# Kernel optimization log

Hardware: AMD Instinct MI355X
Metric: run time of the kernel (lower is better)

The kernel has to match this reference:

```python
import jax, jax.numpy as jnp
import numpy as np
from itertools import permutations

NODE, BATCH, DIM, STEP = 32, 64, 32, 8
E = NODE * (NODE - 1)          # 992 directed edges (all ordered pairs)
K = 3                          # edge types
MSG_HID = 64; MSG_OUT = 64; N_HID = 64; PRED_LEN = 8


def setup_inputs() -> dict:
    key = jax.random.key(0)
    ks = jax.random.split(key, 12)
    es = jnp.asarray(np.array(list(permutations(range(NODE), 2))).T, dtype=jnp.int32)  # [2, E]
    x = jax.random.normal(ks[0], (BATCH, NODE, DIM, STEP), jnp.float32)
    z = jax.nn.softmax(jax.random.normal(ks[1], (BATCH, E, K), jnp.float32), axis=-1)
    p = lambda k, shape: jax.random.normal(k, shape, jnp.float32) * 0.1
    return dict(
        x=x, z=z, es=es,
        nodes_mask=jnp.zeros((NODE,), jnp.float32),
        edges_mask=jnp.zeros((E,), jnp.float32),
        mask=jnp.zeros((1,), jnp.float32),
        msg_W1=p(ks[2], (K, 2 * DIM, MSG_HID)), msg_b1=jnp.zeros((K, MSG_HID), jnp.float32),
        msg_W2=p(ks[3], (K, MSG_HID, MSG_OUT)), msg_b2=jnp.zeros((K, MSG_OUT), jnp.float32),
        out_W1=p(ks[4], (DIM + MSG_OUT, N_HID)), out_b1=jnp.zeros((N_HID,), jnp.float32),
        out_W2=p(ks[5], (N_HID, N_HID)), out_b2=jnp.zeros((N_HID,), jnp.float32),
        out_W3=p(ks[6], (N_HID, DIM)), out_b3=jnp.zeros((DIM,), jnp.float32),
        ge_Wi=p(ks[7], (3, N_HID, N_HID)), ge_bi=jnp.zeros((3, N_HID), jnp.float32),
        ge_Wh=p(ks[8], (3, N_HID, N_HID)), ge_bh=jnp.zeros((3, N_HID), jnp.float32),
        gn_Wi=p(ks[9], (3, N_HID + DIM, N_HID + DIM)), gn_bi=jnp.zeros((3, N_HID + DIM), jnp.float32),
        gn_Wh=p(ks[10], (3, N_HID + DIM, N_HID + DIM)), gn_bh=jnp.zeros((3, N_HID + DIM), jnp.float32),
    )


def _gru(inp, hid, Wi, bi, Wh, bh):
    # GRUX: state defaults to hidden
    r = jax.nn.sigmoid(inp @ Wi[0] + bi[0] + hid @ Wh[0] + bh[0])
    i = jax.nn.sigmoid(inp @ Wi[1] + bi[1] + hid @ Wh[1] + bh[1])
    n = jnp.tanh(inp @ Wi[2] + bi[2] + r * (hid @ Wh[2] + bh[2]))
    return (1.0 - i) * n + i * hid


def _run(x, z, es, msg_W1, msg_b1, msg_W2, msg_b2,
         out_W1, out_b1, out_W2, out_b2, out_W3, out_b3,
         ge_Wi, ge_bi, ge_Wh, ge_bh, gn_Wi, gn_bi, gn_Wh, gn_bh):
    xp = jnp.transpose(x, (1, 0, 3, 2))   # [node, batch, step, dim]
    zp = jnp.transpose(z, (1, 0, 2))      # [E, batch, K]
    col, row = es[0], es[1]               # 'o2i': col,row = es; aggregate at col
    counts = jnp.clip(jax.ops.segment_sum(jnp.ones((E,), x.dtype), col, num_segments=NODE), 1.0)
    h_node = h_edge = None
    x_m = None
    xs = []
    for t in range(STEP + PRED_LEN):
        x_in = xp[:, :, t, :] if t < STEP else x_m   # [node, batch, dim]
        # edge gather: msg = cat([x[row], x[col]])
        msg = jnp.concatenate([x_in[row], x_in[col]], axis=-1)  # [E, b, 2*dim]
        # per-edge-type 2-layer MLP mixture, weighted by z, normalized by K
        h1 = jax.nn.relu(jnp.einsum('ebi,kih->kebh', msg, msg_W1) + msg_b1[:, None, None, :])
        h2 = jax.nn.relu(jnp.einsum('kebh,kho->kebo', h1, msg_W2) + msg_b2[:, None, None, :])
        msgs = jnp.einsum('kebo,ebk->ebo', h2, zp) / K          # [E, b, msg_out]
        if h_edge is not None:
            msgs = _gru(msgs, h_edge, ge_Wi, ge_bi, ge_Wh, ge_bh)
        # scatter-mean to nodes
        agg = jax.ops.segment_sum(msgs, col, num_segments=NODE) / counts[:, None, None]
        cat = jnp.concatenate([x_in, agg], axis=-1)             # [node, b, dim+msg_out]
        if h_node is not None:
            cat = _gru(cat, h_node, gn_Wi, gn_bi, gn_Wh, gn_bh)
        h = jax.nn.relu(cat @ out_W1 + out_b1)
        h = jax.nn.relu(h @ out_W2 + out_b2)
        delta = h @ out_W3 + out_b3
        x_m = x_in + delta
        h_node, h_edge = cat, msgs
        xs.append(x_m)
    x_hat = jnp.transpose(jnp.stack(xs, axis=2), (1, 0, 3, 2))  # [batch, node, dim, T]
    return x_hat


def reference(x, z, es, nodes_mask, edges_mask, mask,
              msg_W1, msg_b1, msg_W2, msg_b2,
              out_W1, out_b1, out_W2, out_b2, out_W3, out_b3,
              ge_Wi, ge_bi, ge_Wh, ge_bh, gn_Wi, gn_bi, gn_Wh, gn_bh):
    x_hat = _run(x, z, es, msg_W1, msg_b1, msg_W2, msg_b2,
                 out_W1, out_b1, out_W2, out_b2, out_W3, out_b3,
                 ge_Wi, ge_bi, ge_Wh, ge_bh, gn_Wi, gn_bi, gn_Wh, gn_bh)
    return (x_hat[:, :, :, -PRED_LEN:], x_hat, x_hat)
```

## Files before the change

kernel.cpp:

```cpp
#include <hip/hip_runtime.h>
#include <hip/hip_bf16.h>

#define NNODE 32
#define NB    64
#define NDIM  32
#define NSTEP 8
#define NE    992
#define NTT   16

typedef __bf16 bf16;
typedef __attribute__((ext_vector_type(8))) __bf16 bf16x8;
typedef __attribute__((ext_vector_type(4))) __bf16 bf16x4;
typedef __attribute__((ext_vector_type(4))) float  f32x4;

__device__ __forceinline__ f32x4 mfma_bf16(bf16x8 a, bf16x8 b, f32x4 c) {
  return __builtin_amdgcn_mfma_f32_16x16x32_bf16(a, b, c, 0, 0, 0);
}
__device__ __forceinline__ float sigm(float x) { return 1.0f / (1.0f + __expf(-x)); }
__device__ __forceinline__ float tanh_f(float x) {
  x = fminf(fmaxf(x, -15.0f), 15.0f);
  float e = __expf(2.0f * x);
  return (e - 1.0f) / (e + 1.0f);
}

__global__ void prep_weights(
    const float* __restrict__ msgW1, const float* __restrict__ msgW2,
    const float* __restrict__ geWi,  const float* __restrict__ geWh,
    const float* __restrict__ gnWi,  const float* __restrict__ gnWh,
    const float* __restrict__ oW1,   const float* __restrict__ oW2,
    const float* __restrict__ oW3,
    bf16* __restrict__ B1, bf16* __restrict__ B2,
    bf16* __restrict__ GI, bf16* __restrict__ GH,
    bf16* __restrict__ GN,
    bf16* __restrict__ OW1s, bf16* __restrict__ OW2s, bf16* __restrict__ OW3s) {
  int u = blockIdx.x * 256 + threadIdx.x;
  if (u < 12288) {
    int k = u >> 12, i = (u >> 6) & 63, h = u & 63;
    int kf = i >> 5, quad = (i >> 3) & 3, j = i & 7;
    int nn = k * 64 + h, nt = nn >> 4, lane = quad * 16 + (nn & 15);
    int slot = ((nt * 2 + kf) * 64 + lane) * 8 + j;
    B1[slot] = (bf16)msgW1[u];
    GI[slot] = (bf16)geWi[u];
    GH[slot] = (bf16)geWh[u];
    int ntl = h >> 4, lane2 = quad * 16 + (h & 15);
    int slot2 = k * 4096 + ((ntl * 2 + kf) * 64 + lane2) * 8 + j;
    B2[slot2] = (bf16)msgW2[u];
  } else if (u < 39936) {
    int v = u - 12288;
    int kk = v / 9216, rem = v % 9216, i = rem / 96, h = rem % 96;
    int kf = i >> 5, loc = i & 31, quad = loc >> 3, j = loc & 7;
    int nn = kk * 96 + h, nt = nn >> 4, lane = quad * 16 + (nn & 15);
    int slot = ((nt * 3 + kf) * 64 + lane) * 8 + j;
    GN[slot]         = (bf16)gnWi[v];
    GN[27648 + slot] = (bf16)gnWh[v];
  } else if (u < 46080) {
    int v = u - 39936; int i = v >> 6, h = v & 63;
    int kf = i >> 5, loc = i & 31, quad = loc >> 3, j = loc & 7;
    int nt = h >> 4, lane = quad * 16 + (h & 15);
    OW1s[((nt * 3 + kf) * 64 + lane) * 8 + j] = (bf16)oW1[v];
  } else if (u < 50176) {
    int v = u - 46080; int i = v >> 6, h = v & 63;
    int kf = i >> 5, quad = (i >> 3) & 3, j = i & 7;
    int nt = h >> 4, lane = quad * 16 + (h & 15);
    OW2s[((nt * 2 + kf) * 64 + lane) * 8 + j] = (bf16)oW2[v];
  } else if (u < 52224) {
    int v = u - 50176; int i = v >> 5, h = v & 31;
    int kf = i >> 5, quad = (i >> 3) & 3, j = i & 7;
    int nt = h >> 4, lane = quad * 16 + (h & 15);
    OW3s[((nt * 2 + kf) * 64 + lane) * 8 + j] = (bf16)oW3[v];
  }
}

__global__ void copy_x(const float* __restrict__ x, float* __restrict__ xf,
                       bf16* __restrict__ xb) {
  int u = blockIdx.x * 256 + threadIdx.x;
  int n = u >> 11, b = (u >> 5) & 63, d = u & 31;
  float v = x[((b * 32 + n) * 32 + d) * 8 + 0];
  xf[u] = v;
  xb[u] = (bf16)v;
}

__global__ __launch_bounds__(256, 2) void edge_step(
    const bf16* __restrict__ xb, const int* __restrict__ es,
    const float* __restrict__ z,
    const bf16* __restrict__ B1, const bf16* __restrict__ B2,
    const float* __restrict__ mb1, const float* __restrict__ mb2,
    const bf16* __restrict__ GI, const bf16* __restrict__ GH,
    const float* __restrict__ gbi, const float* __restrict__ gbh,
    bf16* __restrict__ hed, int t) {
  __shared__ __align__(16) char scrbuf[51200];
  __shared__ float zL[2][64][3];
  __shared__ float biasL[768];
  bf16 (*A)[64][72]   = (bf16(*)[64][72])scrbuf;
  bf16 (*A2)[64][200] = (bf16(*)[64][200])scrbuf;

  int e0 = blockIdx.x * 2, tid = threadIdx.x;
  int c0_ = es[e0],     r0 = es[NE + e0];
  int c1_ = es[e0 + 1], r1 = es[NE + e0 + 1];
  for (int u = tid; u < 768; u += 256)
    biasL[u] = (u < 192) ? mb1[u] : (u < 384) ? mb2[u - 192]
             : (u < 576) ? gbi[u - 384] : gbh[u - 576];
  for (int u = tid; u < 384; u += 256) {
    int pe = u / 192, rem = u % 192, b = rem / 3, k = rem % 3;
    zL[pe][b][k] = z[(b * NE + e0 + pe) * 3 + k];
  }
  for (int u = tid; u < 1024; u += 256) {
    int pe = u >> 9, c = u & 511;
    int b = c >> 3, i8 = c & 7;
    int nrow = pe ? r1 : r0, ncol = pe ? c1_ : c0_;
    const bf16* src = (i8 < 4) ? (xb + nrow * 2048 + b * 32 + i8 * 8)
                               : (xb + ncol * 2048 + b * 32 + (i8 - 4) * 8);
    *(bf16x8*)&A[pe][b][i8 * 8] = *(const bf16x8*)src;
  }
  __syncthreads();
  int wv = tid >> 6, ln = tid & 63, quad = ln >> 4, l16 = ln & 15;
  int m = wv * 16 + l16;
  bf16x8 af[2][2];
#pragma unroll
  for (int pe = 0; pe < 2; pe++)
#pragma unroll
    for (int kf = 0; kf < 2; kf++)
      af[pe][kf] = *(const bf16x8*)&A[pe][m][kf * 32 + quad * 8];
  __syncthreads();
  f32x4 acc[2][12];
#pragma unroll
  for (int pe = 0; pe < 2; pe++)
#pragma unroll
    for (int q = 0; q < 12; q++) { f32x4 zz = {0.f,0.f,0.f,0.f}; acc[pe][q] = zz; }
#pragma unroll
  for (int nt = 0; nt < 12; nt++) {
    bf16x8 w0 = *(const bf16x8*)&B1[(nt * 2 + 0) * 512 + ln * 8];
    bf16x8 w1 = *(const bf16x8*)&B1[(nt * 2 + 1) * 512 + ln * 8];
#pragma unroll
    for (int pe = 0; pe < 2; pe++) {
      acc[pe][nt] = mfma_bf16(af[pe][0], w0, acc[pe][nt]);
      acc[pe][nt] = mfma_bf16(af[pe][1], w1, acc[pe][nt]);
    }
  }
#pragma unroll
  for (int nt = 0; nt < 12; nt++) {
    int n = nt * 16 + l16;
    float bias = biasL[n];
#pragma unroll
    for (int pe = 0; pe < 2; pe++)
#pragma unroll
      for (int r = 0; r < 4; r++) {
        float v = acc[pe][nt][r] + bias;
        A2[pe][wv * 16 + quad * 4 + r][n] = (bf16)(v > 0.f ? v : 0.f);
      }
  }
  __syncthreads();
  bf16x8 a2[2][3][2];
#pragma unroll
  for (int pe = 0; pe < 2; pe++)
#pragma unroll
    for (int kt = 0; kt < 3; kt++)
#pragma unroll
      for (int kf = 0; kf < 2; kf++)
        a2[pe][kt][kf] = *(const bf16x8*)&A2[pe][m][kt * 64 + kf * 32 + quad * 8];
  __syncthreads();
  f32x4 acc2[2][12];
#pragma unroll
  for (int pe = 0; pe < 2; pe++)
#pragma unroll
    for (int q = 0; q < 12; q++) { f32x4 zz = {0.f,0.f,0.f,0.f}; acc2[pe][q] = zz; }
#pragma unroll
  for (int kt = 0; kt < 3; kt++)
#pragma unroll
    for (int nt = 0; nt < 4; nt++) {
      bf16x8 w0 = *(const bf16x8*)&B2[kt * 4096 + (nt * 2 + 0) * 512 + ln * 8];
      bf16x8 w1 = *(const bf16x8*)&B2[kt * 4096 + (nt * 2 + 1) * 512 + ln * 8];
#pragma unroll
      for (int pe = 0; pe < 2; pe++) {
        acc2[pe][kt * 4 + nt] = mfma_bf16(a2[pe][kt][0], w0, acc2[pe][kt * 4 + nt]);
        acc2[pe][kt * 4 + nt] = mfma_bf16(a2[pe][kt][1], w1, acc2[pe][kt * 4 + nt]);
      }
    }
#pragma unroll
  for (int pe = 0; pe < 2; pe++)
#pragma unroll
    for (int r = 0; r < 4; r++) {
      int b = wv * 16 + quad * 4 + r;
      float z0 = zL[pe][b][0], z1 = zL[pe][b][1], z2 = zL[pe][b][2];
#pragma unroll
      for (int nt = 0; nt < 4; nt++) {
        int o = nt * 16 + l16;
        float h0 = acc2[pe][nt][r]     + biasL[192 + o];       h0 = h0 > 0.f ? h0 : 0.f;
        float h1 = acc2[pe][4 + nt][r] + biasL[192 + 64 + o];  h1 = h1 > 0.f ? h1 : 0.f;
        float h2 = acc2[pe][8 + nt][r] + biasL[192 + 128 + o]; h2 = h2 > 0.f ? h2 : 0.f;
        A[pe][b][o] = (bf16)((h0 * z0 + h1 * z1 + h2 * z2) * (1.0f / 3.0f));
      }
    }
  if (t > 0) {
    __syncthreads();
    bf16x8 ai[2][2], ah[2][2];
#pragma unroll
    for (int pe = 0; pe < 2; pe++) {
      const bf16* hrow = hed + (e0 + pe) * 4096 + m * 64;
#pragma unroll
      for (int kf = 0; kf < 2; kf++) {
        ai[pe][kf] = *(const bf16x8*)&A[pe][m][kf * 32 + quad * 8];
        ah[pe][kf] = *(const bf16x8*)(hrow + kf * 32 + quad * 8);
      }
    }
    f32x4 gri[2][8], gni[2][4], gnh[2][4];
#pragma unroll
    for (int pe = 0; pe < 2; pe++) {
#pragma unroll
      for (int q = 0; q < 8; q++) { f32x4 zz = {0.f,0.f,0.f,0.f}; gri[pe][q] = zz; }
#pragma unroll
      for (int q = 0; q < 4; q++) { f32x4 zz = {0.f,0.f,0.f,0.f}; gni[pe][q] = zz; gnh[pe][q] = zz; }
    }
#pragma unroll
    for (int nt = 0; nt < 8; nt++) {
      bf16x8 wi0 = *(const bf16x8*)&GI[(nt * 2 + 0) * 512 + ln * 8];
      bf16x8 wi1 = *(const bf16x8*)&GI[(nt * 2 + 1) * 512 + ln * 8];
      bf16x8 wh0 = *(const bf16x8*)&GH[(nt * 2 + 0) * 512 + ln * 8];
      bf16x8 wh1 = *(const bf16x8*)&GH[(nt * 2 + 1) * 512 + ln * 8];
#pragma unroll
      for (int pe = 0; pe < 2; pe++) {
        gri[pe][nt] = mfma_bf16(ai[pe][0], wi0, gri[pe][nt]);
        gri[pe][nt] = mfma_bf16(ai[pe][1], wi1, gri[pe][nt]);
        gri[pe][nt] = mfma_bf16(ah[pe][0], wh0, gri[pe][nt]);
        gri[pe][nt] = mfma_bf16(ah[pe][1], wh1, gri[pe][nt]);
      }
    }
#pragma unroll
    for (int nt = 8; nt < 12; nt++) {
      bf16x8 wi0 = *(const bf16x8*)&GI[(nt * 2 + 0) * 512 + ln * 8];
      bf16x8 wi1 = *(const bf16x8*)&GI[(nt * 2 + 1) * 512 + ln * 8];
      bf16x8 wh0 = *(const bf16x8*)&GH[(nt * 2 + 0) * 512 + ln * 8];
      bf16x8 wh1 = *(const bf16x8*)&GH[(nt * 2 + 1) * 512 + ln * 8];
#pragma unroll
      for (int pe = 0; pe < 2; pe++) {
        gni[pe][nt - 8] = mfma_bf16(ai[pe][0], wi0, gni[pe][nt - 8]);
        gni[pe][nt - 8] = mfma_bf16(ai[pe][1], wi1, gni[pe][nt - 8]);
        gnh[pe][nt - 8] = mfma_bf16(ah[pe][0], wh0, gnh[pe][nt - 8]);
        gnh[pe][nt - 8] = mfma_bf16(ah[pe][1], wh1, gnh[pe][nt - 8]);
      }
    }
#pragma unroll
    for (int pe = 0; pe < 2; pe++)
#pragma unroll
      for (int r = 0; r < 4; r++) {
        int b = wv * 16 + quad * 4 + r;
#pragma unroll
        for (int nt = 0; nt < 4; nt++) {
          int o = nt * 16 + l16;
          float xr = gri[pe][nt][r]     + biasL[384 + o]      + biasL[576 + o];
          float xi = gri[pe][4 + nt][r] + biasL[384 + 64 + o] + biasL[576 + 64 + o];
          float xn = gni[pe][nt][r] + biasL[384 + 128 + o];
          float hn = gnh[pe][nt][r] + biasL[576 + 128 + o];
          float rg = sigm(xr);
          float ig = sigm(xi);
          float ng = tanh_f(xn + rg * hn);
          float hv = (float)hed[(e0 + pe) * 4096 + b * 64 + o];
          A[pe][b][o] = (bf16)((1.0f - ig) * ng + ig * hv);
        }
      }
  }
  __syncthreads();
  for (int u = tid; u < 1024; u += 256) {
    int pe = u >> 9, c = u & 511;
    int b = c >> 3, j = c & 7;
    *(bf16x8*)(hed + (e0 + pe) * 4096 + b * 64 + j * 8) = *(const bf16x8*)&A[pe][b][j * 8];
  }
}

__global__ __launch_bounds__(256) void node_kernel(
    const float* __restrict__ x, const bf16* __restrict__ hed,
    float* __restrict__ xf, bf16* __restrict__ xb, float* __restrict__ hnode,
    const bf16* __restrict__ GN,
    const float* __restrict__ gnbi, const float* __restrict__ gnbh,
    const bf16* __restrict__ OW1, const float* __restrict__ ob1,
    const bf16* __restrict__ OW2, const float* __restrict__ ob2,
    const bf16* __restrict__ OW3, const float* __restrict__ ob3,
    float* __restrict__ out, int t) {
  __shared__ float aggf[16][64];
  __shared__ float xinf[16][32];
  __shared__ float hvf[16][96];
  __shared__ __align__(16) bf16 c0b[16][112];
  __shared__ __align__(16) bf16 hvb[16][112];
  __shared__ float gsum[2][16][290];
  __shared__ __align__(16) bf16 cnb[16][112];
  __shared__ __align__(16) bf16 s1b[16][112];
  __shared__ __align__(16) bf16 s2b[16][112];
  int nq = blockIdx.x, n = nq >> 2, q = nq & 3;
  int tid = threadIdx.x;
  {
    int r = tid >> 4, o4 = tid & 15;
    const bf16x4* bp = (const bf16x4*)hed + (size_t)n * 31 * 1024 + (q * 16 + r) * 16 + o4;
    float sx = 0.f, sy = 0.f, sz = 0.f, sw = 0.f;
#pragma unroll
    for (int e2 = 0; e2 < 31; e2++) {
      bf16x4 v = bp[e2 * 1024];
      sx += (float)v[0]; sy += (float)v[1]; sz += (float)v[2]; sw += (float)v[3];
    }
    const float inv = 1.0f / 31.0f;
    sx *= inv; sy *= inv; sz *= inv; sw *= inv;
    int o = o4 * 4;
    aggf[r][o] = sx; aggf[r][o + 1] = sy; aggf[r][o + 2] = sz; aggf[r][o + 3] = sw;
    c0b[r][32 + o] = (bf16)sx; c0b[r][33 + o] = (bf16)sy;
    c0b[r][34 + o] = (bf16)sz; c0b[r][35 + o] = (bf16)sw;
  }
  if (tid < 128) {
    int r = tid >> 3, d0 = (tid & 7) * 4;
    int b = q * 16 + r;
#pragma unroll
    for (int k = 0; k < 4; k++) {
      float v = xf[n * 2048 + b * 32 + d0 + k];
      xinf[r][d0 + k] = v;
      c0b[r][d0 + k] = (bf16)v;
    }
  }
  if (t > 0) {
    int r = tid >> 4, cb = (tid & 15) * 6;
    int row = n * 64 + q * 16 + r;
#pragma unroll
    for (int k = 0; k < 6; k++) {
      float v = hnode[row * 96 + cb + k];
      hvf[r][cb + k] = v;
      hvb[r][cb + k] = (bf16)v;
    }
  }
  __syncthreads();
  int wv = tid >> 6, ln = tid & 63, quad = ln >> 4, l16 = ln & 15;
  if (t > 0) {
    int mat = wv >> 1, sel = wv & 1;
    const bf16(*Ab)[112] = mat ? hvb : c0b;
    bf16x8 af[3];
#pragma unroll
    for (int kf = 0; kf < 3; kf++)
      af[kf] = *(const bf16x8*)&Ab[l16][kf * 32 + quad * 8];
    const bf16* W = GN + mat * 27648;
    f32x4 accn[9];
#pragma unroll
    for (int q2 = 0; q2 < 9; q2++) { f32x4 zz = {0.f,0.f,0.f,0.f}; accn[q2] = zz; }
#pragma unroll
    for (int nt2 = 0; nt2 < 9; nt2++) {
      int nt = sel * 9 + nt2;
#pragma unroll
      for (int kf = 0; kf < 3; kf++) {
        bf16x8 bfrag = *(const bf16x8*)&W[((nt * 3 + kf) * 64 + ln) * 8];
        accn[nt2] = mfma_bf16(af[kf], bfrag, accn[nt2]);
      }
    }
#pragma unroll
    for (int nt2 = 0; nt2 < 9; nt2++) {
      int col = (sel * 9 + nt2) * 16 + l16;
#pragma unroll
      for (int rr = 0; rr < 4; rr++)
        gsum[mat][quad * 4 + rr][col] = accn[nt2][rr];
    }
  }
  __syncthreads();
  {
    int r = tid >> 4, cb = (tid & 15) * 6;
    int row = n * 64 + q * 16 + r;
#pragma unroll
    for (int k = 0; k < 6; k++) {
      int c = cb + k;
      float v;
      if (t > 0) {
        float xr = gsum[0][r][c] + gnbi[c] + gsum[1][r][c] + gnbh[c];
        float xi = gsum[0][r][96 + c] + gnbi[96 + c] + gsum[1][r][96 + c] + gnbh[96 + c];
        float xn = gsum[0][r][192 + c] + gnbi[192 + c];
        float hn = gsum[1][r][192 + c] + gnbh[192 + c];
        float rg = sigm(xr);
        float ig = sigm(xi);
        float ng = tanh_f(xn + rg * hn);
        v = (1.0f - ig) * ng + ig * hvf[r][c];
      } else {
        v = (c < 32) ? xinf[r][c] : aggf[r][c - 32];
      }
      cnb[r][c] = (bf16)v;
      hnode[row * 96 + c] = v;
    }
  }
  __syncthreads();
  {
    bf16x8 af[3];
#pragma unroll
    for (int kf = 0; kf < 3; kf++)
      af[kf] = *(const bf16x8*)&cnb[l16][kf * 32 + quad * 8];
    f32x4 accn = {0.f, 0.f, 0.f, 0.f};
#pragma unroll
    for (int kf = 0; kf < 3; kf++) {
      bf16x8 bfrag = *(const bf16x8*)&OW1[((wv * 3 + kf) * 64 + ln) * 8];
      accn = mfma_bf16(af[kf], bfrag, accn);
    }
    int col = wv * 16 + l16;
    float bias = ob1[col];
#pragma unroll
    for (int rr = 0; rr < 4; rr++) {
      float vv = accn[rr] + bias;
      s1b[quad * 4 + rr][col] = (bf16)(vv > 0.f ? vv : 0.f);
    }
  }
  __syncthreads();
  {
    bf16x8 af[2];
#pragma unroll
    for (int kf = 0; kf < 2; kf++)
      af[kf] = *(const bf16x8*)&s1b[l16][kf * 32 + quad * 8];
    f32x4 accn = {0.f, 0.f, 0.f, 0.f};
#pragma unroll
    for (int kf = 0; kf < 2; kf++) {
      bf16x8 bfrag = *(const bf16x8*)&OW2[((wv * 2 + kf) * 64 + ln) * 8];
      accn = mfma_bf16(af[kf], bfrag, accn);
    }
    int col = wv * 16 + l16;
    float bias = ob2[col];
#pragma unroll
    for (int rr = 0; rr < 4; rr++) {
      float vv = accn[rr] + bias;
      s2b[quad * 4 + rr][col] = (bf16)(vv > 0.f ? vv : 0.f);
    }
  }
  __syncthreads();
  if (wv < 2) {
    bf16x8 af[2];
#pragma unroll
    for (int kf = 0; kf < 2; kf++)
      af[kf] = *(const bf16x8*)&s2b[l16][kf * 32 + quad * 8];
    f32x4 accn = {0.f, 0.f, 0.f, 0.f};
#pragma unroll
    for (int kf = 0; kf < 2; kf++) {
      bf16x8 bfrag = *(const bf16x8*)&OW3[((wv * 2 + kf) * 64 + ln) * 8];
      accn = mfma_bf16(af[kf], bfrag, accn);
    }
    int d = wv * 16 + l16;
    float bias = ob3[d];
#pragma unroll
    for (int rr = 0; rr < 4; rr++) {
      int r = quad * 4 + rr;
      int b = q * 16 + r;
      float xm = xinf[r][d] + accn[rr] + bias;
      int base = (b * 32 + n) * 32 + d;
      out[524288 + base * 16 + t] = xm;
      out[1572864 + base * 16 + t] = xm;
      if (t >= NSTEP) out[base * 8 + (t - NSTEP)] = xm;
      float vnext = (t + 1 < NSTEP) ? x[base * 8 + (t + 1)] : xm;
      xf[n * 2048 + b * 32 + d] = vnext;
      xb[n * 2048 + b * 32 + d] = (bf16)vnext;
    }
  }
}

extern "C" void kernel_launch(void* const* d_in, const int* in_sizes, int n_in,
                              void* d_out, int out_size, void* d_ws, size_t ws_size,
                              hipStream_t stream) {
  const float* x     = (const float*)d_in[0];
  const float* z     = (const float*)d_in[1];
  const int*   es    = (const int*)d_in[2];
  const float* msgW1 = (const float*)d_in[6];
  const float* msgb1 = (const float*)d_in[7];
  const float* msgW2 = (const float*)d_in[8];
  const float* msgb2 = (const float*)d_in[9];
  const float* oW1   = (const float*)d_in[10];
  const float* ob1   = (const float*)d_in[11];
  const float* oW2   = (const float*)d_in[12];
  const float* ob2   = (const float*)d_in[13];
  const float* oW3   = (const float*)d_in[14];
  const float* ob3   = (const float*)d_in[15];
  const float* geWi  = (const float*)d_in[16];
  const float* gebi  = (const float*)d_in[17];
  const float* geWh  = (const float*)d_in[18];
  const float* gebh  = (const float*)d_in[19];
  const float* gnWi  = (const float*)d_in[20];
  const float* gnbi  = (const float*)d_in[21];
  const float* gnWh  = (const float*)d_in[22];
  const float* gnbh  = (const float*)d_in[23];
  float* out = (float*)d_out;

  char* p = (char*)d_ws;
  bf16*  hed   = (bf16*)p;   p += (size_t)NE * 4096 * 2;
  float* xf    = (float*)p;  p += 65536 * 4;
  bf16*  xb    = (bf16*)p;   p += 65536 * 2;
  float* hnode = (float*)p;  p += 196608 * 4;
  bf16*  B1sw  = (bf16*)p;   p += 12288 * 2;
  bf16*  B2sw  = (bf16*)p;   p += 12288 * 2;
  bf16*  GIsw  = (bf16*)p;   p += 12288 * 2;
  bf16*  GHsw  = (bf16*)p;   p += 12288 * 2;
  bf16*  GNsw  = (bf16*)p;   p += 55296 * 2;
  bf16*  OW1s  = (bf16*)p;   p += 6144 * 2;
  bf16*  OW2s  = (bf16*)p;   p += 4096 * 2;
  bf16*  OW3s  = (bf16*)p;   p += 2048 * 2;

  prep_weights<<<204, 256, 0, stream>>>(msgW1, msgW2, geWi, geWh, gnWi, gnWh,
                                        oW1, oW2, oW3,
                                        B1sw, B2sw, GIsw, GHsw, GNsw,
                                        OW1s, OW2s, OW3s);
  copy_x<<<256, 256, 0, stream>>>(x, xf, xb);

  for (int t = 0; t < NTT; t++) {
    edge_step<<<NE / 2, 256, 0, stream>>>(xb, es, z, B1sw, B2sw, msgb1, msgb2,
                                          GIsw, GHsw, gebi, gebh, hed, t);
    node_kernel<<<128, 256, 0, stream>>>(x, hed, xf, xb, hnode, GNsw, gnbi, gnbh,
                                         OW1s, ob1, OW2s, ob2, OW3s, ob3,
                                         out, t);
  }
}
```

Measured before the change: 658.2 us.

## Precompute per-node first-layer message projections instead of per-edge GEMM

```diff
diff --git a/kernel.cpp b/kernel.cpp
--- a/kernel.cpp
+++ b/kernel.cpp
@@ -29,7 +29,7 @@
     const float* __restrict__ gnWi,  const float* __restrict__ gnWh,
     const float* __restrict__ oW1,   const float* __restrict__ oW2,
     const float* __restrict__ oW3,
-    bf16* __restrict__ B1, bf16* __restrict__ B2,
+    bf16* __restrict__ W1P, bf16* __restrict__ B2,
     bf16* __restrict__ GI, bf16* __restrict__ GH,
     bf16* __restrict__ GN,
     bf16* __restrict__ OW1s, bf16* __restrict__ OW2s, bf16* __restrict__ OW3s) {
@@ -39,12 +39,15 @@
     int kf = i >> 5, quad = (i >> 3) & 3, j = i & 7;
     int nn = k * 64 + h, nt = nn >> 4, lane = quad * 16 + (nn & 15);
     int slot = ((nt * 2 + kf) * 64 + lane) * 8 + j;
-    B1[slot] = (bf16)msgW1[u];
     GI[slot] = (bf16)geWi[u];
     GH[slot] = (bf16)geWh[u];
     int ntl = h >> 4, lane2 = quad * 16 + (h & 15);
     int slot2 = k * 4096 + ((ntl * 2 + kf) * 64 + lane2) * 8 + j;
     B2[slot2] = (bf16)msgW2[u];
+    int loc = i & 31, q3 = loc >> 3, j3 = loc & 7;
+    int nt3 = kf * 12 + (nn >> 4);
+    int lane3 = q3 * 16 + (nn & 15);
+    W1P[(nt3 * 64 + lane3) * 8 + j3] = (bf16)msgW1[u];
   } else if (u < 39936) {
     int v = u - 12288;
     int kk = v / 9216, rem = v % 9216, i = rem / 96, h = rem % 96;
@@ -71,32 +74,68 @@
   }
 }
 
-__global__ void copy_x(const float* __restrict__ x, float* __restrict__ xf,
-                       bf16* __restrict__ xb) {
+__global__ void copy_x0(const float* __restrict__ x, float* __restrict__ xf) {
   int u = blockIdx.x * 256 + threadIdx.x;
   int n = u >> 11, b = (u >> 5) & 63, d = u & 31;
-  float v = x[((b * 32 + n) * 32 + d) * 8 + 0];
-  xf[u] = v;
-  xb[u] = (bf16)v;
+  xf[u] = x[((b * 32 + n) * 32 + d) * 8 + 0];
+}
+
+__global__ __launch_bounds__(256) void p8_kernel(
+    const float* __restrict__ x, const bf16* __restrict__ W1P,
+    float* __restrict__ Pbuf) {
+  __shared__ __align__(16) bf16 XA[64][40];
+  int t = blockIdx.x >> 5, n = blockIdx.x & 31;
+  int tid = threadIdx.x;
+  for (int u = tid; u < 2048; u += 256) {
+    int b = u >> 5, d = u & 31;
+    XA[b][d] = (bf16)x[((b * 32 + n) * 32 + d) * 8 + t];
+  }
+  __syncthreads();
+  int wv = tid >> 6, ln = tid & 63, quad = ln >> 4, l16 = ln & 15;
+  bf16x8 a = *(const bf16x8*)&XA[wv * 16 + l16][quad * 8];
+  float* Pt = Pbuf + ((size_t)(t * 32 + n) * 64) * 384;
+#pragma unroll
+  for (int nt = 0; nt < 24; nt++) {
+    bf16x8 bfr = *(const bf16x8*)&W1P[(nt * 64 + ln) * 8];
+    f32x4 c = {0.f, 0.f, 0.f, 0.f};
+    c = mfma_bf16(a, bfr, c);
+#pragma unroll
+    for (int rr = 0; rr < 4; rr++)
+      Pt[(size_t)(wv * 16 + quad * 4 + rr) * 384 + nt * 16 + l16] = c[rr];
+  }
+}
+
+__device__ __forceinline__ bf16x8 mk_h1(const float* b1p, const float* b2p,
+                                        const float* biasL, int col) {
+  f32x4 pa0 = *(const f32x4*)(b1p + col);
+  f32x4 pa1 = *(const f32x4*)(b1p + col + 4);
+  f32x4 pb0 = *(const f32x4*)(b2p + col);
+  f32x4 pb1 = *(const f32x4*)(b2p + col + 4);
+  bf16x8 h;
+#pragma unroll
+  for (int j = 0; j < 4; j++) {
+    float v0 = pa0[j] + pb0[j] + biasL[col + j];
+    float v1 = pa1[j] + pb1[j] + biasL[col + 4 + j];
+    h[j]     = (bf16)(v0 > 0.f ? v0 : 0.f);
+    h[4 + j] = (bf16)(v1 > 0.f ? v1 : 0.f);
+  }
+  return h;
 }
 
 __global__ __launch_bounds__(256, 2) void edge_step(
-    const bf16* __restrict__ xb, const int* __restrict__ es,
+    const float* __restrict__ P, const int* __restrict__ es,
     const float* __restrict__ z,
-    const bf16* __restrict__ B1, const bf16* __restrict__ B2,
+    const bf16* __restrict__ B2,
     const float* __restrict__ mb1, const float* __restrict__ mb2,
     const bf16* __restrict__ GI, const bf16* __restrict__ GH,
     const float* __restrict__ gbi, const float* __restrict__ gbh,
-    bf16* __restrict__ hed, int t) {
-  __shared__ __align__(16) char scrbuf[51200];
+    bf16* __restrict__ hed, int do_gru) {
+  __shared__ __align__(16) bf16 S[2][64][72];
   __shared__ float zL[2][64][3];
   __shared__ float biasL[768];
-  bf16 (*A)[64][72]   = (bf16(*)[64][72])scrbuf;
-  bf16 (*A2)[64][200] = (bf16(*)[64][200])scrbuf;
-
   int e0 = blockIdx.x * 2, tid = threadIdx.x;
-  int c0_ = es[e0],     r0 = es[NE + e0];
-  int c1_ = es[e0 + 1], r1 = es[NE + e0 + 1];
+  int cn0 = es[e0], rn0 = es[NE + e0];
+  int cn1 = es[e0 + 1], rn1 = es[NE + e0 + 1];
   for (int u = tid; u < 768; u += 256)
     biasL[u] = (u < 192) ? mb1[u] : (u < 384) ? mb2[u - 192]
              : (u < 576) ? gbi[u - 384] : gbh[u - 576];
@@ -104,61 +143,21 @@
     int pe = u / 192, rem = u % 192, b = rem / 3, k = rem % 3;
     zL[pe][b][k] = z[(b * NE + e0 + pe) * 3 + k];
   }
-  for (int u = tid; u < 1024; u += 256) {
-    int pe = u >> 9, c = u & 511;
-    int b = c >> 3, i8 = c & 7;
-    int nrow = pe ? r1 : r0, ncol = pe ? c1_ : c0_;
-    const bf16* src = (i8 < 4) ? (xb + nrow * 2048 + b * 32 + i8 * 8)
-                               : (xb + ncol * 2048 + b * 32 + (i8 - 4) * 8);
-    *(bf16x8*)&A[pe][b][i8 * 8] = *(const bf16x8*)src;
-  }
   __syncthreads();
   int wv = tid >> 6, ln = tid & 63, quad = ln >> 4, l16 = ln & 15;
   int m = wv * 16 + l16;
-  bf16x8 af[2][2];
-#pragma unroll
-  for (int pe = 0; pe < 2; pe++)
-#pragma unroll
-    for (int kf = 0; kf < 2; kf++)
-      af[pe][kf] = *(const bf16x8*)&A[pe][m][kf * 32 + quad * 8];
-  __syncthreads();
-  f32x4 acc[2][12];
-#pragma unroll
-  for (int pe = 0; pe < 2; pe++)
-#pragma unroll
-    for (int q = 0; q < 12; q++) { f32x4 zz = {0.f,0.f,0.f,0.f}; acc[pe][q] = zz; }
-#pragma unroll
-  for (int nt = 0; nt < 12; nt++) {
-    bf16x8 w0 = *(const bf16x8*)&B1[(nt * 2 + 0) * 512 + ln * 8];
-    bf16x8 w1 = *(const bf16x8*)&B1[(nt * 2 + 1) * 512 + ln * 8];
-#pragma unroll
-    for (int pe = 0; pe < 2; pe++) {
-      acc[pe][nt] = mfma_bf16(af[pe][0], w0, acc[pe][nt]);
-      acc[pe][nt] = mfma_bf16(af[pe][1], w1, acc[pe][nt]);
-    }
-  }
-#pragma unroll
-  for (int nt = 0; nt < 12; nt++) {
-    int n = nt * 16 + l16;
-    float bias = biasL[n];
-#pragma unroll
-    for (int pe = 0; pe < 2; pe++)
-#pragma unroll
-      for (int r = 0; r < 4; r++) {
-        float v = acc[pe][nt][r] + bias;
-        A2[pe][wv * 16 + quad * 4 + r][n] = (bf16)(v > 0.f ? v : 0.f);
-      }
-  }
-  __syncthreads();
   bf16x8 a2[2][3][2];
 #pragma unroll
-  for (int pe = 0; pe < 2; pe++)
+  for (int pe = 0; pe < 2; pe++) {
+    int rn = pe ? rn1 : rn0, cnn = pe ? cn1 : cn0;
+    const float* b1p = P + ((size_t)rn * 64 + m) * 384;
+    const float* b2p = P + ((size_t)cnn * 64 + m) * 384 + 192;
 #pragma unroll
     for (int kt = 0; kt < 3; kt++)
 #pragma unroll
       for (int kf = 0; kf < 2; kf++)
-        a2[pe][kt][kf] = *(const bf16x8*)&A2[pe][m][kt * 64 + kf * 32 + quad * 8];
-  __syncthreads();
+        a2[pe][kt][kf] = mk_h1(b1p, b2p, biasL, kt * 64 + kf * 32 + quad * 8);
+  }
   f32x4 acc2[2][12];
 #pragma unroll
   for (int pe = 0; pe < 2; pe++)
@@ -188,18 +187,18 @@
         float h0 = acc2[pe][nt][r]     + biasL[192 + o];       h0 = h0 > 0.f ? h0 : 0.f;
         float h1 = acc2[pe][4 + nt][r] + biasL[192 + 64 + o];  h1 = h1 > 0.f ? h1 : 0.f;
         float h2 = acc2[pe][8 + nt][r] + biasL[192 + 128 + o]; h2 = h2 > 0.f ? h2 : 0.f;
-        A[pe][b][o] = (bf16)((h0 * z0 + h1 * z1 + h2 * z2) * (1.0f / 3.0f));
-      }
-    }
-  if (t > 0) {
+        S[pe][b][o] = (bf16)((h0 * z0 + h1 * z1 + h2 * z2) * (1.0f / 3.0f));
+      }
+    }
+  if (do_gru) {
     __syncthreads();
     bf16x8 ai[2][2], ah[2][2];
 #pragma unroll
     for (int pe = 0; pe < 2; pe++) {
-      const bf16* hrow = hed + (e0 + pe) * 4096 + m * 64;
+      const bf16* hrow = hed + (size_t)(e0 + pe) * 4096 + m * 64;
 #pragma unroll
       for (int kf = 0; kf < 2; kf++) {
-        ai[pe][kf] = *(const bf16x8*)&A[pe][m][kf * 32 + quad * 8];
+        ai[pe][kf] = *(const bf16x8*)&S[pe][m][kf * 32 + quad * 8];
         ah[pe][kf] = *(const bf16x8*)(hrow + kf * 32 + quad * 8);
       }
     }
@@ -254,27 +253,27 @@
           float rg = sigm(xr);
           float ig = sigm(xi);
           float ng = tanh_f(xn + rg * hn);
-          float hv = (float)hed[(e0 + pe) * 4096 + b * 64 + o];
-          A[pe][b][o] = (bf16)((1.0f - ig) * ng + ig * hv);
+          float hv = (float)hed[(size_t)(e0 + pe) * 4096 + b * 64 + o];
+          S[pe][b][o] = (bf16)((1.0f - ig) * ng + ig * hv);
         }
       }
   }
   __syncthreads();
   for (int u = tid; u < 1024; u += 256) {
-    int pe = u >> 9, c = u & 511;
-    int b = c >> 3, j = c & 7;
-    *(bf16x8*)(hed + (e0 + pe) * 4096 + b * 64 + j * 8) = *(const bf16x8*)&A[pe][b][j * 8];
+    int pe = u >> 9, c = u & 511, b = c >> 3, j = c & 7;
+    *(bf16x8*)(hed + (size_t)(e0 + pe) * 4096 + b * 64 + j * 8) = *(const bf16x8*)&S[pe][b][j * 8];
   }
 }
 
 __global__ __launch_bounds__(256) void node_kernel(
     const float* __restrict__ x, const bf16* __restrict__ hed,
-    float* __restrict__ xf, bf16* __restrict__ xb, float* __restrict__ hnode,
+    float* __restrict__ xf, float* __restrict__ hnode,
     const bf16* __restrict__ GN,
     const float* __restrict__ gnbi, const float* __restrict__ gnbh,
     const bf16* __restrict__ OW1, const float* __restrict__ ob1,
     const bf16* __restrict__ OW2, const float* __restrict__ ob2,
     const bf16* __restrict__ OW3, const float* __restrict__ ob3,
+    const bf16* __restrict__ W1P, float* __restrict__ Pcur,
     float* __restrict__ out, int t) {
   __shared__ float aggf[16][64];
   __shared__ float xinf[16][32];
@@ -285,6 +284,7 @@
   __shared__ __align__(16) bf16 cnb[16][112];
   __shared__ __align__(16) bf16 s1b[16][112];
   __shared__ __align__(16) bf16 s2b[16][112];
+  __shared__ __align__(16) bf16 xnb[16][40];
   int nq = blockIdx.x, n = nq >> 2, q = nq & 3;
   int tid = threadIdx.x;
   {
@@ -442,7 +442,21 @@
       if (t >= NSTEP) out[base * 8 + (t - NSTEP)] = xm;
       float vnext = (t + 1 < NSTEP) ? x[base * 8 + (t + 1)] : xm;
       xf[n * 2048 + b * 32 + d] = vnext;
-      xb[n * 2048 + b * 32 + d] = (bf16)vnext;
+      xnb[r][d] = (bf16)vnext;
+    }
+  }
+  __syncthreads();
+  if (t + 1 >= NSTEP && t + 1 < NTT) {
+    bf16x8 a = *(const bf16x8*)&xnb[l16][quad * 8];
+#pragma unroll
+    for (int s = 0; s < 6; s++) {
+      int nt = wv * 6 + s;
+      bf16x8 bfr = *(const bf16x8*)&W1P[(nt * 64 + ln) * 8];
+      f32x4 c = {0.f, 0.f, 0.f, 0.f};
+      c = mfma_bf16(a, bfr, c);
+#pragma unroll
+      for (int rr = 0; rr < 4; rr++)
+        Pcur[(size_t)(n * 64 + q * 16 + quad * 4 + rr) * 384 + nt * 16 + l16] = c[rr];
     }
   }
 }
@@ -475,10 +489,11 @@
 
   char* p = (char*)d_ws;
   bf16*  hed   = (bf16*)p;   p += (size_t)NE * 4096 * 2;
+  float* Pbuf  = (float*)p;  p += (size_t)8 * 32 * 64 * 384 * 4;
+  float* Pcur  = (float*)p;  p += (size_t)32 * 64 * 384 * 4;
   float* xf    = (float*)p;  p += 65536 * 4;
-  bf16*  xb    = (bf16*)p;   p += 65536 * 2;
   float* hnode = (float*)p;  p += 196608 * 4;
-  bf16*  B1sw  = (bf16*)p;   p += 12288 * 2;
+  bf16*  W1Psw = (bf16*)p;   p += 12288 * 2;
   bf16*  B2sw  = (bf16*)p;   p += 12288 * 2;
   bf16*  GIsw  = (bf16*)p;   p += 12288 * 2;
   bf16*  GHsw  = (bf16*)p;   p += 12288 * 2;
@@ -489,15 +504,17 @@
 
   prep_weights<<<204, 256, 0, stream>>>(msgW1, msgW2, geWi, geWh, gnWi, gnWh,
                                         oW1, oW2, oW3,
-                                        B1sw, B2sw, GIsw, GHsw, GNsw,
+                                        W1Psw, B2sw, GIsw, GHsw, GNsw,
                                         OW1s, OW2s, OW3s);
-  copy_x<<<256, 256, 0, stream>>>(x, xf, xb);
+  copy_x0<<<256, 256, 0, stream>>>(x, xf);
+  p8_kernel<<<256, 256, 0, stream>>>(x, W1Psw, Pbuf);
 
   for (int t = 0; t < NTT; t++) {
-    edge_step<<<NE / 2, 256, 0, stream>>>(xb, es, z, B1sw, B2sw, msgb1, msgb2,
-                                          GIsw, GHsw, gebi, gebh, hed, t);
-    node_kernel<<<128, 256, 0, stream>>>(x, hed, xf, xb, hnode, GNsw, gnbi, gnbh,
+    const float* Pt = (t < NSTEP) ? (Pbuf + (size_t)t * 32 * 64 * 384) : Pcur;
+    edge_step<<<496, 256, 0, stream>>>(Pt, es, z, B2sw, msgb1, msgb2,
+                                       GIsw, GHsw, gebi, gebh, hed, t > 0 ? 1 : 0);
+    node_kernel<<<128, 256, 0, stream>>>(x, hed, xf, hnode, GNsw, gnbi, gnbh,
                                          OW1s, ob1, OW2s, ob2, OW3s, ob3,
-                                         out, t);
-  }
-}
+                                         W1Psw, Pcur, out, t);
+  }
+}
```

After: 829.4 us. 26.0% more time.
